# Optimization experiments

Hardware: AMD Instinct MI355X
Metric: run time of the kernel (lower is better)

Reference implementation:

```python
import jax, jax.numpy as jnp
import numpy as np

B, T, C, H = 8, 2048, 1024, 64  # batch, time(block_size), n_embd, head_size


def setup_inputs() -> dict:
    key = jax.random.key(0)
    k1, k2, k3, k4 = jax.random.split(key, 4)
    x = jax.random.normal(k1, (B, T, C), dtype=jnp.float32)
    # nn.Linear(n_embd, head_size, bias=False): y = x @ W.T with W [H, C];
    # store as [C, H] so projection is x @ W.
    Wq = jax.random.normal(k2, (C, H), dtype=jnp.float32) * 0.02
    Wk = jax.random.normal(k3, (C, H), dtype=jnp.float32) * 0.02
    Wv = jax.random.normal(k4, (C, H), dtype=jnp.float32) * 0.02
    return {"x": x, "Wq": Wq, "Wk": Wk, "Wv": Wv}


def reference(x, Wq, Wk, Wv):
    # x: [B, T, C]
    Bb, Tt, Cc = x.shape
    q = x @ Wq  # [B, T, H]
    k = x @ Wk  # [B, T, H]
    v = x @ Wv  # [B, T, H]
    # scores = Q @ K^T / sqrt(channels)  -- note: code scales by n_embd, not head_size
    scale = jnp.asarray(Cc, x.dtype) ** 0.5
    scores = jnp.einsum('bth,bsh->bts', q, k) / scale  # [B, T, T]
    # causal mask (decoder=True): lower-triangular allowed
    causal = jnp.tril(jnp.ones((Tt, Tt), dtype=bool))
    scores = jnp.where(causal, scores, -jnp.inf)
    attn = jax.nn.softmax(scores, axis=-1)  # [B, T, T]
    # dropout p=0.0 -> identity
    res = attn @ v  # [B, T, H]
    return res, attn
```

## Files before the change

### kernel.cpp

```cpp
#include <hip/hip_runtime.h>
#include <hip/hip_bf16.h>


typedef __attribute__((ext_vector_type(8))) short bf16x8;
typedef __attribute__((ext_vector_type(4))) float f32x4;

#define NB 8
#define NT 2048
#define NC 1024
#define NH 64

__device__ __forceinline__ unsigned short f2bf(float f) {
    unsigned int u = __builtin_bit_cast(unsigned int, f);
    u += 0x7fffu + ((u >> 16) & 1u);
    return (unsigned short)(u >> 16);
}

__device__ __forceinline__ bf16x8 cvt8(float4 a, float4 b) {
    union { bf16x8 v; __hip_bfloat162 h[4]; } u;
    u.h[0] = __float22bfloat162_rn(make_float2(a.x, a.y));
    u.h[1] = __float22bfloat162_rn(make_float2(a.z, a.w));
    u.h[2] = __float22bfloat162_rn(make_float2(b.x, b.y));
    u.h[3] = __float22bfloat162_rn(make_float2(b.z, b.w));
    return u.v;
}

__device__ __forceinline__ void async_ld16(const void* g, const void* l) {
    __builtin_amdgcn_global_load_lds(
        (const __attribute__((address_space(1))) unsigned int*)g,
        (__attribute__((address_space(3))) unsigned int*)(unsigned int)(unsigned long long)l,
        16, 0, 0);
}

__global__ __launch_bounds__(256) void wt_kernel(
        const float* __restrict__ Wq,
        const float* __restrict__ Wk,
        const float* __restrict__ Wv,
        unsigned short* __restrict__ Wt) {
    __shared__ float tile[64][65];
    int m  = blockIdx.x >> 4;
    int k0 = (blockIdx.x & 15) * 64;
    const float* W = (m == 0) ? Wq : ((m == 1) ? Wk : Wv);
    int tid = threadIdx.x;
    for (int i = 0; i < 4; ++i) {
        int f = tid + i * 256;
        int r = f >> 4, c4 = (f & 15) * 4;
        float4 v = *(const float4*)&W[(size_t)(k0 + r) * 64 + c4];
        tile[r][c4 + 0] = v.x; tile[r][c4 + 1] = v.y;
        tile[r][c4 + 2] = v.z; tile[r][c4 + 3] = v.w;
    }
    __syncthreads();
    int n  = tid & 63;
    int kq = (tid >> 6) * 16;
    float scale = (m == 0) ? 0.03125f : 1.0f;
    __attribute__((aligned(16))) unsigned short outv[16];
    for (int j = 0; j < 16; ++j)
        outv[j] = f2bf(tile[kq + j][n] * scale);
    unsigned short* dst = &Wt[(size_t)m * (64 * 1024) + (size_t)n * 1024 + k0 + kq];
    *(uint4*)dst       = *(const uint4*)&outv[0];
    *(uint4*)(dst + 8) = *(const uint4*)&outv[8];
}

__global__ __launch_bounds__(256) void qkv_kernel(
        const float* __restrict__ x,
        const unsigned short* __restrict__ Wt,
        unsigned short* __restrict__ qkv,
        unsigned short* __restrict__ v_t) {
    __shared__ float At[32 * 64];
    __shared__ unsigned short Bt[192 * 64];
    char* Ab = (char*)At;
    char* Bb = (char*)Bt;

    int tid  = threadIdx.x;
    int wave = tid >> 6, lane = tid & 63, quad = lane >> 4, l15 = lane & 15;
    int row0 = blockIdx.x * 32;

    f32x4 acc[2][3];
#pragma unroll
    for (int rt = 0; rt < 2; ++rt)
#pragma unroll
        for (int j = 0; j < 3; ++j) acc[rt][j] = (f32x4){0.f, 0.f, 0.f, 0.f};

    for (int kb = 0; kb < 16; ++kb) {
        __syncthreads();
#pragma unroll
        for (int i = 0; i < 2; ++i) {
            int s = i * 256 + tid;
            int m = s >> 4, p = s & 15;
            int j = (p & 8) | ((p & 7) ^ (m & 7));
            async_ld16(x + (size_t)(row0 + m) * NC + kb * 64 + j * 4,
                       Ab + i * 4096 + wave * 1024);
        }
#pragma unroll
        for (int i = 0; i < 6; ++i) {
            int s = i * 256 + tid;
            int n = s >> 3, p = s & 7;
            int j = p ^ (n & 7);
            async_ld16(Wt + (size_t)n * NC + kb * 64 + j * 8,
                       Bb + i * 4096 + wave * 1024);
        }
        __syncthreads();

#pragma unroll
        for (int c = 0; c < 2; ++c) {
            bf16x8 af[2];
#pragma unroll
            for (int rt = 0; rt < 2; ++rt) {
                int m  = rt * 16 + l15;
                int j0 = c * 8 + quad * 2;
                int p0 = (j0 & 8) | ((j0 & 7) ^ (m & 7));
                int p1 = (j0 & 8) | (((j0 + 1) & 7) ^ (m & 7));
                float4 a0 = *(const float4*)(Ab + m * 256 + p0 * 16);
                float4 a1 = *(const float4*)(Ab + m * 256 + p1 * 16);
                af[rt] = cvt8(a0, a1);
            }
#pragma unroll
            for (int jj = 0; jj < 3; ++jj) {
                int n = (wave * 3 + jj) * 16 + l15;
                int p = (c * 4 + quad) ^ (n & 7);
                bf16x8 bf = *(const bf16x8*)(Bb + n * 128 + p * 16);
#pragma unroll
                for (int rt = 0; rt < 2; ++rt)
                    acc[rt][jj] = __builtin_amdgcn_mfma_f32_16x16x32_bf16(
                        af[rt], bf, acc[rt][jj], 0, 0, 0);
            }
        }
    }

    int b = row0 >> 11;
#pragma unroll
    for (int jj = 0; jj < 3; ++jj) {
        int g   = wave * 3 + jj;
        int mat = g >> 2;
        int col = (g & 3) * 16 + l15;
#pragma unroll
        for (int rt = 0; rt < 2; ++rt) {
            int rowb = row0 + rt * 16 + quad * 4;
            if (mat < 2) {
#pragma unroll
                for (int r = 0; r < 4; ++r)
                    qkv[(size_t)mat * (16384 * 64) + (size_t)(rowb + r) * 64 + col] =
                        f2bf(acc[rt][jj][r]);
            } else {
                union { unsigned long long q; unsigned short us[4]; } pk;
#pragma unroll
                for (int r = 0; r < 4; ++r) pk.us[r] = f2bf(acc[rt][jj][r]);
                *(unsigned long long*)&v_t[((size_t)b * 64 + col) * NT + (rowb & 2047)] = pk.q;
            }
        }
    }
}

__global__ __launch_bounds__(256) void lsum_kernel(
        const unsigned short* __restrict__ qg,
        const unsigned short* __restrict__ kg,
        float* __restrict__ l) {
    __shared__ unsigned short kt[64 * 64];
    char* ktb = (char*)kt;
    int tid  = threadIdx.x;
    int wave = tid >> 6, lane = tid & 63, quad = lane >> 4, l15 = lane & 15;
    int it = blockIdx.x >> 2, qq = blockIdx.x & 3;
    int b  = blockIdx.y;
    if (qq > it) return;
    int t0 = it * 64;
    size_t brow = (size_t)b * NT;

    bf16x8 qf[2];
    {
        const unsigned short* qp = qg + (brow + t0 + wave * 16 + l15) * NH + quad * 8;
        qf[0] = *(const bf16x8*)qp;
        qf[1] = *(const bf16x8*)(qp + 32);
    }
    int trow[4];
#pragma unroll
    for (int r = 0; r < 4; ++r) trow[r] = t0 + wave * 16 + quad * 4 + r;

    float rs[4] = {0.f, 0.f, 0.f, 0.f};

    for (int st = qq; st <= it; st += 4) {
        __syncthreads();
#pragma unroll
        for (int i = 0; i < 2; ++i) {
            int s = i * 256 + tid;
            int r = s >> 3, p = s & 7;
            int j = p ^ (r & 7);
            async_ld16(kg + (brow + st * 64 + r) * NH + j * 8,
                       ktb + i * 4096 + wave * 1024);
        }
        __syncthreads();

        f32x4 sacc[4];
#pragma unroll
        for (int nt = 0; nt < 4; ++nt) sacc[nt] = (f32x4){0.f, 0.f, 0.f, 0.f};
#pragma unroll
        for (int c = 0; c < 2; ++c)
#pragma unroll
            for (int nt = 0; nt < 4; ++nt) {
                int n = nt * 16 + l15;
                int p = (c * 4 + quad) ^ (n & 7);
                bf16x8 kf = *(const bf16x8*)(ktb + n * 128 + p * 16);
                sacc[nt] = __builtin_amdgcn_mfma_f32_16x16x32_bf16(qf[c], kf, sacc[nt], 0, 0, 0);
            }
        bool dia = (st == it);
#pragma unroll
        for (int nt = 0; nt < 4; ++nt) {
            int s_g = st * 64 + nt * 16 + l15;
#pragma unroll
            for (int r = 0; r < 4; ++r) {
                float e = __expf(sacc[nt][r]);
                if (dia && s_g > trow[r]) e = 0.f;
                rs[r] += e;
            }
        }
    }
#pragma unroll
    for (int r = 0; r < 4; ++r) {
        float v = rs[r];
        v += __shfl_xor(v, 1, 16);
        v += __shfl_xor(v, 2, 16);
        v += __shfl_xor(v, 4, 16);
        v += __shfl_xor(v, 8, 16);
        if (l15 == 0)
            unsafeAtomicAdd(&l[brow + trow[r]], v);
    }
}

__global__ __launch_bounds__(256) void attn_m_kernel(
        const unsigned short* __restrict__ qg,
        const unsigned short* __restrict__ kg,
        const unsigned short* __restrict__ vtg,
        const float* __restrict__ l,
        float* __restrict__ res,
        float* __restrict__ attn) {
    __shared__ unsigned short kt[64 * 64];
    __shared__ unsigned short vt[64 * 64];
    __shared__ float ptf[4 * 16 * 68];
    char* ktb = (char*)kt;
    char* vtb = (char*)vt;

    int tid  = threadIdx.x;
    int wave = tid >> 6, lane = tid & 63, quad = lane >> 4, l15 = lane & 15;
    int it = blockIdx.x >> 2, qq = blockIdx.x & 3;
    int b  = blockIdx.y;
    if (qq > it) return;
    int t0 = it * 64;
    size_t brow = (size_t)b * NT;

    bf16x8 qf[2];
    {
        const unsigned short* qp = qg + (brow + t0 + wave * 16 + l15) * NH + quad * 8;
        qf[0] = *(const bf16x8*)qp;
        qf[1] = *(const bf16x8*)(qp + 32);
    }
    int trow[4];
    float rinv[4];
#pragma unroll
    for (int r = 0; r < 4; ++r) {
        trow[r] = t0 + wave * 16 + quad * 4 + r;
        rinv[r] = 1.0f / l[brow + trow[r]];
    }

    f32x4 oacc[4];
#pragma unroll
    for (int nt = 0; nt < 4; ++nt) oacc[nt] = (f32x4){0.f, 0.f, 0.f, 0.f};

    for (int st = qq; st <= it; st += 4) {
        __syncthreads();
#pragma unroll
        for (int i = 0; i < 2; ++i) {
            int s = i * 256 + tid;
            int r = s >> 3, p = s & 7;
            int j = p ^ (r & 7);
            async_ld16(kg + (brow + st * 64 + r) * NH + j * 8,
                       ktb + i * 4096 + wave * 1024);
        }
#pragma unroll
        for (int i = 0; i < 2; ++i) {
            int s = i * 256 + tid;
            int r = s >> 3, p = s & 7;
            int j = p ^ (r & 7);
            async_ld16(vtg + ((size_t)b * 64 + r) * NT + st * 64 + j * 8,
                       vtb + i * 4096 + wave * 1024);
        }
        __syncthreads();

        f32x4 sacc[4];
#pragma unroll
        for (int nt = 0; nt < 4; ++nt) sacc[nt] = (f32x4){0.f, 0.f, 0.f, 0.f};
#pragma unroll
        for (int c = 0; c < 2; ++c)
#pragma unroll
            for (int nt = 0; nt < 4; ++nt) {
                int n = nt * 16 + l15;
                int p = (c * 4 + quad) ^ (n & 7);
                bf16x8 kf = *(const bf16x8*)(ktb + n * 128 + p * 16);
                sacc[nt] = __builtin_amdgcn_mfma_f32_16x16x32_bf16(qf[c], kf, sacc[nt], 0, 0, 0);
            }

        bool dia = (st == it);
#pragma unroll
        for (int nt = 0; nt < 4; ++nt) {
            int s_g = st * 64 + nt * 16 + l15;
#pragma unroll
            for (int r = 0; r < 4; ++r) {
                float p = __expf(sacc[nt][r]) * rinv[r];
                if (dia && s_g > trow[r]) p = 0.f;
                ptf[wave * 1088 + (quad * 4 + r) * 68 + nt * 16 + l15] = p;
            }
        }
        asm volatile("s_waitcnt lgkmcnt(0)" ::: "memory");

#pragma unroll
        for (int r = 0; r < 4; ++r) {
            int row = quad * 4 + r;
            float4 pv = *(const float4*)&ptf[wave * 1088 + row * 68 + l15 * 4];
            *(float4*)&attn[(brow + t0 + wave * 16 + row) * NT + st * 64 + l15 * 4] = pv;
        }

#pragma unroll
        for (int c = 0; c < 2; ++c) {
            const float* pp = &ptf[wave * 1088 + l15 * 68 + c * 32 + quad * 8];
            float4 a0 = *(const float4*)pp;
            float4 a1 = *(const float4*)(pp + 4);
            bf16x8 pf = cvt8(a0, a1);
#pragma unroll
            for (int nt = 0; nt < 4; ++nt) {
                int n = nt * 16 + l15;
                int p = (c * 4 + quad) ^ (n & 7);
                bf16x8 vf = *(const bf16x8*)(vtb + n * 128 + p * 16);
                oacc[nt] = __builtin_amdgcn_mfma_f32_16x16x32_bf16(pf, vf, oacc[nt], 0, 0, 0);
            }
        }
    }

#pragma unroll
    for (int nt = 0; nt < 4; ++nt)
#pragma unroll
        for (int r = 0; r < 4; ++r)
            unsafeAtomicAdd(&res[(brow + trow[r]) * NH + nt * 16 + l15], oacc[nt][r]);
}

__global__ __launch_bounds__(256) void zero_kernel(float* __restrict__ attn) {
    int lt = blockIdx.x, b = blockIdx.y;
    float fr = sqrtf(8.f * (float)lt + 1.f);
    int i = (int)((fr + 1.f) * 0.5f);
    while (i * (i - 1) / 2 > lt) --i;
    while ((i + 1) * i / 2 <= lt) ++i;
    int j = lt - i * (i - 1) / 2;
    int it = j, st = i;
    size_t brow = (size_t)b * NT;
    int t0 = it * 64;
    float4 z4 = {0.f, 0.f, 0.f, 0.f};
    int tid = threadIdx.x;
    for (int k = 0; k < 4; ++k) {
        int f = tid + k * 256;
        int r = f >> 4, c4 = (f & 15) * 4;
        *(float4*)&attn[(brow + t0 + r) * NT + st * 64 + c4] = z4;
    }
}

extern "C" void kernel_launch(void* const* d_in, const int* in_sizes, int n_in,
                              void* d_out, int out_size, void* d_ws, size_t ws_size,
                              hipStream_t stream) {
    const float* x  = (const float*)d_in[0];
    const float* Wq = (const float*)d_in[1];
    const float* Wk = (const float*)d_in[2];
    const float* Wv = (const float*)d_in[3];

    unsigned short* ws  = (unsigned short*)d_ws;
    unsigned short* Wt  = ws;
    unsigned short* qkv = ws + 3 * 64 * 1024;
    unsigned short* v_t = qkv + 2 * 16384 * 64;
    float* l = (float*)(v_t + 16384 * 64);

    float* res  = (float*)d_out;
    float* attn = res + (size_t)NB * NT * NH;

    hipMemsetAsync(l, 0, (size_t)NB * NT * sizeof(float), stream);
    hipMemsetAsync(res, 0, (size_t)NB * NT * NH * sizeof(float), stream);

    hipLaunchKernelGGL(wt_kernel, dim3(48), dim3(256), 0, stream, Wq, Wk, Wv, Wt);
    hipLaunchKernelGGL(qkv_kernel, dim3(512), dim3(256), 0, stream, x, Wt, qkv, v_t);

    const unsigned short* qg = qkv;
    const unsigned short* kg = qkv + 16384 * 64;

    hipLaunchKernelGGL(lsum_kernel, dim3(128, 8), dim3(256), 0, stream, qg, kg, l);
    hipLaunchKernelGGL(attn_m_kernel, dim3(128, 8), dim3(256), 0, stream,
                       qg, kg, v_t, l, res, attn);
    hipLaunchKernelGGL(zero_kernel, dim3(496, 8), dim3(256), 0, stream, attn);
}
```

Before: 229.6 us.

## Fuse row-sum and attention passes, normalize attn and output in finalize kernel

Merges the separate row-sum pass and the attention pass into one kernel that writes unnormalized exp scores to attn, accumulates P@V unnormalized, and atomically adds row sums. A new finalize kernel reads the attn lower triangle back, scales it by the inverse row sum, zeros the upper triangle and rescales the output rows. This removes the repeated QK^T and exp work, but adds a full read-modify-write of the lower-triangular attn matrix in global memory. It also relies on no max subtraction, which the previous code already assumed.

```diff
diff --git a/kernel.cpp b/kernel.cpp
--- a/kernel.cpp
+++ b/kernel.cpp
@@ -151,12 +151,19 @@
     }
 }
 
-__global__ __launch_bounds__(256) void lsum_kernel(
+__global__ __launch_bounds__(256) void attn_u_kernel(
         const unsigned short* __restrict__ qg,
         const unsigned short* __restrict__ kg,
-        float* __restrict__ l) {
+        const unsigned short* __restrict__ vtg,
+        float* __restrict__ l,
+        float* __restrict__ res,
+        float* __restrict__ attn) {
     __shared__ unsigned short kt[64 * 64];
+    __shared__ unsigned short vt[64 * 64];
+    __shared__ float ptf[4 * 16 * 68];
     char* ktb = (char*)kt;
+    char* vtb = (char*)vt;
+
     int tid  = threadIdx.x;
     int wave = tid >> 6, lane = tid & 63, quad = lane >> 4, l15 = lane & 15;
     int it = blockIdx.x >> 2, qq = blockIdx.x & 3;
@@ -175,6 +182,9 @@
 #pragma unroll
     for (int r = 0; r < 4; ++r) trow[r] = t0 + wave * 16 + quad * 4 + r;
 
+    f32x4 oacc[4];
+#pragma unroll
+    for (int nt = 0; nt < 4; ++nt) oacc[nt] = (f32x4){0.f, 0.f, 0.f, 0.f};
     float rs[4] = {0.f, 0.f, 0.f, 0.f};
 
     for (int st = qq; st <= it; st += 4) {
@@ -187,6 +197,14 @@
             async_ld16(kg + (brow + st * 64 + r) * NH + j * 8,
                        ktb + i * 4096 + wave * 1024);
         }
+#pragma unroll
+        for (int i = 0; i < 2; ++i) {
+            int s = i * 256 + tid;
+            int r = s >> 3, p = s & 7;
+            int j = p ^ (r & 7);
+            async_ld16(vtg + ((size_t)b * 64 + r) * NT + st * 64 + j * 8,
+                       vtb + i * 4096 + wave * 1024);
+        }
         __syncthreads();
 
         f32x4 sacc[4];
@@ -201,6 +219,7 @@
                 bf16x8 kf = *(const bf16x8*)(ktb + n * 128 + p * 16);
                 sacc[nt] = __builtin_amdgcn_mfma_f32_16x16x32_bf16(qf[c], kf, sacc[nt], 0, 0, 0);
             }
+
         bool dia = (st == it);
 #pragma unroll
         for (int nt = 0; nt < 4; ++nt) {
@@ -210,9 +229,34 @@
                 float e = __expf(sacc[nt][r]);
                 if (dia && s_g > trow[r]) e = 0.f;
                 rs[r] += e;
-            }
-        }
-    }
+                ptf[wave * 1088 + (quad * 4 + r) * 68 + nt * 16 + l15] = e;
+            }
+        }
+        asm volatile("s_waitcnt lgkmcnt(0)" ::: "memory");
+
+#pragma unroll
+        for (int r = 0; r < 4; ++r) {
+            int row = quad * 4 + r;
+            float4 pv = *(const float4*)&ptf[wave * 1088 + row * 68 + l15 * 4];
+            *(float4*)&attn[(brow + t0 + wave * 16 + row) * NT + st * 64 + l15 * 4] = pv;
+        }
+
+#pragma unroll
+        for (int c = 0; c < 2; ++c) {
+            const float* pp = &ptf[wave * 1088 + l15 * 68 + c * 32 + quad * 8];
+            float4 a0 = *(const float4*)pp;
+            float4 a1 = *(const float4*)(pp + 4);
+            bf16x8 pf = cvt8(a0, a1);
+#pragma unroll
+            for (int nt = 0; nt < 4; ++nt) {
+                int n = nt * 16 + l15;
+                int p = (c * 4 + quad) ^ (n & 7);
+                bf16x8 vf = *(const bf16x8*)(vtb + n * 128 + p * 16);
+                oacc[nt] = __builtin_amdgcn_mfma_f32_16x16x32_bf16(pf, vf, oacc[nt], 0, 0, 0);
+            }
+        }
+    }
+
 #pragma unroll
     for (int r = 0; r < 4; ++r) {
         float v = rs[r];
@@ -223,139 +267,62 @@
         if (l15 == 0)
             unsafeAtomicAdd(&l[brow + trow[r]], v);
     }
-}
-
-__global__ __launch_bounds__(256) void attn_m_kernel(
-        const unsigned short* __restrict__ qg,
-        const unsigned short* __restrict__ kg,
-        const unsigned short* __restrict__ vtg,
+
+#pragma unroll
+    for (int nt = 0; nt < 4; ++nt)
+#pragma unroll
+        for (int r = 0; r < 4; ++r)
+            unsafeAtomicAdd(&res[(brow + trow[r]) * NH + nt * 16 + l15], oacc[nt][r]);
+}
+
+__global__ __launch_bounds__(256) void finalize_kernel(
         const float* __restrict__ l,
         float* __restrict__ res,
         float* __restrict__ attn) {
-    __shared__ unsigned short kt[64 * 64];
-    __shared__ unsigned short vt[64 * 64];
-    __shared__ float ptf[4 * 16 * 68];
-    char* ktb = (char*)kt;
-    char* vtb = (char*)vt;
-
-    int tid  = threadIdx.x;
-    int wave = tid >> 6, lane = tid & 63, quad = lane >> 4, l15 = lane & 15;
-    int it = blockIdx.x >> 2, qq = blockIdx.x & 3;
+    __shared__ float rinv[64];
+    int bx = blockIdx.x;
+    int it = bx >> 5, st = bx & 31;
     int b  = blockIdx.y;
-    if (qq > it) return;
-    int t0 = it * 64;
-    size_t brow = (size_t)b * NT;
-
-    bf16x8 qf[2];
-    {
-        const unsigned short* qp = qg + (brow + t0 + wave * 16 + l15) * NH + quad * 8;
-        qf[0] = *(const bf16x8*)qp;
-        qf[1] = *(const bf16x8*)(qp + 32);
-    }
-    int trow[4];
-    float rinv[4];
-#pragma unroll
-    for (int r = 0; r < 4; ++r) {
-        trow[r] = t0 + wave * 16 + quad * 4 + r;
-        rinv[r] = 1.0f / l[brow + trow[r]];
-    }
-
-    f32x4 oacc[4];
-#pragma unroll
-    for (int nt = 0; nt < 4; ++nt) oacc[nt] = (f32x4){0.f, 0.f, 0.f, 0.f};
-
-    for (int st = qq; st <= it; st += 4) {
-        __syncthreads();
-#pragma unroll
-        for (int i = 0; i < 2; ++i) {
-            int s = i * 256 + tid;
-            int r = s >> 3, p = s & 7;
-            int j = p ^ (r & 7);
-            async_ld16(kg + (brow + st * 64 + r) * NH + j * 8,
-                       ktb + i * 4096 + wave * 1024);
-        }
-#pragma unroll
-        for (int i = 0; i < 2; ++i) {
-            int s = i * 256 + tid;
-            int r = s >> 3, p = s & 7;
-            int j = p ^ (r & 7);
-            async_ld16(vtg + ((size_t)b * 64 + r) * NT + st * 64 + j * 8,
-                       vtb + i * 4096 + wave * 1024);
-        }
-        __syncthreads();
-
-        f32x4 sacc[4];
-#pragma unroll
-        for (int nt = 0; nt < 4; ++nt) sacc[nt] = (f32x4){0.f, 0.f, 0.f, 0.f};
-#pragma unroll
-        for (int c = 0; c < 2; ++c)
-#pragma unroll
-            for (int nt = 0; nt < 4; ++nt) {
-                int n = nt * 16 + l15;
-                int p = (c * 4 + quad) ^ (n & 7);
-                bf16x8 kf = *(const bf16x8*)(ktb + n * 128 + p * 16);
-                sacc[nt] = __builtin_amdgcn_mfma_f32_16x16x32_bf16(qf[c], kf, sacc[nt], 0, 0, 0);
-            }
-
-        bool dia = (st == it);
-#pragma unroll
-        for (int nt = 0; nt < 4; ++nt) {
-            int s_g = st * 64 + nt * 16 + l15;
-#pragma unroll
-            for (int r = 0; r < 4; ++r) {
-                float p = __expf(sacc[nt][r]) * rinv[r];
-                if (dia && s_g > trow[r]) p = 0.f;
-                ptf[wave * 1088 + (quad * 4 + r) * 68 + nt * 16 + l15] = p;
-            }
-        }
-        asm volatile("s_waitcnt lgkmcnt(0)" ::: "memory");
-
-#pragma unroll
-        for (int r = 0; r < 4; ++r) {
-            int row = quad * 4 + r;
-            float4 pv = *(const float4*)&ptf[wave * 1088 + row * 68 + l15 * 4];
-            *(float4*)&attn[(brow + t0 + wave * 16 + row) * NT + st * 64 + l15 * 4] = pv;
-        }
-
-#pragma unroll
-        for (int c = 0; c < 2; ++c) {
-            const float* pp = &ptf[wave * 1088 + l15 * 68 + c * 32 + quad * 8];
-            float4 a0 = *(const float4*)pp;
-            float4 a1 = *(const float4*)(pp + 4);
-            bf16x8 pf = cvt8(a0, a1);
-#pragma unroll
-            for (int nt = 0; nt < 4; ++nt) {
-                int n = nt * 16 + l15;
-                int p = (c * 4 + quad) ^ (n & 7);
-                bf16x8 vf = *(const bf16x8*)(vtb + n * 128 + p * 16);
-                oacc[nt] = __builtin_amdgcn_mfma_f32_16x16x32_bf16(pf, vf, oacc[nt], 0, 0, 0);
-            }
-        }
-    }
-
-#pragma unroll
-    for (int nt = 0; nt < 4; ++nt)
-#pragma unroll
-        for (int r = 0; r < 4; ++r)
-            unsafeAtomicAdd(&res[(brow + trow[r]) * NH + nt * 16 + l15], oacc[nt][r]);
-}
-
-__global__ __launch_bounds__(256) void zero_kernel(float* __restrict__ attn) {
-    int lt = blockIdx.x, b = blockIdx.y;
-    float fr = sqrtf(8.f * (float)lt + 1.f);
-    int i = (int)((fr + 1.f) * 0.5f);
-    while (i * (i - 1) / 2 > lt) --i;
-    while ((i + 1) * i / 2 <= lt) ++i;
-    int j = lt - i * (i - 1) / 2;
-    int it = j, st = i;
     size_t brow = (size_t)b * NT;
     int t0 = it * 64;
-    float4 z4 = {0.f, 0.f, 0.f, 0.f};
     int tid = threadIdx.x;
+
+    if (st > it) {
+        float4 z4 = {0.f, 0.f, 0.f, 0.f};
+#pragma unroll
+        for (int k = 0; k < 4; ++k) {
+            int f = tid + k * 256;
+            int r = f >> 4, c4 = (f & 15) * 4;
+            *(float4*)&attn[(brow + t0 + r) * NT + st * 64 + c4] = z4;
+        }
+        return;
+    }
+
+    if (tid < 64) rinv[tid] = 1.0f / l[brow + t0 + tid];
+    __syncthreads();
+
+#pragma unroll
     for (int k = 0; k < 4; ++k) {
         int f = tid + k * 256;
         int r = f >> 4, c4 = (f & 15) * 4;
-        *(float4*)&attn[(brow + t0 + r) * NT + st * 64 + c4] = z4;
+        float* p = &attn[(brow + t0 + r) * NT + st * 64 + c4];
+        float4 v = *(const float4*)p;
+        float s = rinv[r];
+        v.x *= s; v.y *= s; v.z *= s; v.w *= s;
+        *(float4*)p = v;
+    }
+
+    if (st == it) {
+#pragma unroll
+        for (int k = 0; k < 4; ++k) {
+            int f = tid + k * 256;
+            int r = f >> 4, c4 = (f & 15) * 4;
+            float* p = &res[(brow + t0 + r) * NH + c4];
+            float4 v = *(const float4*)p;
+            float s = rinv[r];
+            v.x *= s; v.y *= s; v.z *= s; v.w *= s;
+            *(float4*)p = v;
+        }
     }
 }
 
@@ -385,8 +352,8 @@
     const unsigned short* qg = qkv;
     const unsigned short* kg = qkv + 16384 * 64;
 
-    hipLaunchKernelGGL(lsum_kernel, dim3(128, 8), dim3(256), 0, stream, qg, kg, l);
-    hipLaunchKernelGGL(attn_m_kernel, dim3(128, 8), dim3(256), 0, stream,
+    hipLaunchKernelGGL(attn_u_kernel, dim3(128, 8), dim3(256), 0, stream,
                        qg, kg, v_t, l, res, attn);
-    hipLaunchKernelGGL(zero_kernel, dim3(496, 8), dim3(256), 0, stream, attn);
-}
+    hipLaunchKernelGGL(finalize_kernel, dim3(1024, 8), dim3(256), 0, stream,
+                       l, res, attn);
+}
```

Result: slower. 236.3 us (+2.9%).

## Double-buffer LDS tiles in QKV, row-sum and attention kernels

Applied to the files above, without the earlier changes.

Adds two-stage LDS ping-pong buffering to the QKV projection, the softmax row-sum and the attention output kernels. The next K/V (or x/W) tile is prefetched with async global-to-LDS loads while the current tile feeds the MFMAs, and the second barrier per iteration is dropped. The aim is to hide global load latency behind matrix math. In exchange, LDS use doubles (64 KB per block in the QKV kernel), which can lower occupancy. The full vmcnt(0) drain also waits on outstanding attn stores.

```diff
diff --git a/kernel.cpp b/kernel.cpp
--- a/kernel.cpp
+++ b/kernel.cpp
@@ -9,6 +9,8 @@
 #define NT 2048
 #define NC 1024
 #define NH 64
+
+#define VM_DRAIN() asm volatile("s_waitcnt vmcnt(0)" ::: "memory")
 
 __device__ __forceinline__ unsigned short f2bf(float f) {
     unsigned int u = __builtin_bit_cast(unsigned int, f);
@@ -66,10 +68,7 @@
         const unsigned short* __restrict__ Wt,
         unsigned short* __restrict__ qkv,
         unsigned short* __restrict__ v_t) {
-    __shared__ float At[32 * 64];
-    __shared__ unsigned short Bt[192 * 64];
-    char* Ab = (char*)At;
-    char* Bb = (char*)Bt;
+    __shared__ char smem[65536];
 
     int tid  = threadIdx.x;
     int wave = tid >> 6, lane = tid & 63, quad = lane >> 4, l15 = lane & 15;
@@ -81,26 +80,48 @@
 #pragma unroll
         for (int j = 0; j < 3; ++j) acc[rt][j] = (f32x4){0.f, 0.f, 0.f, 0.f};
 
+#pragma unroll
+    for (int i = 0; i < 2; ++i) {
+        int s = i * 256 + tid;
+        int m = s >> 4, p = s & 15;
+        int j = (p & 8) | ((p & 7) ^ (m & 7));
+        async_ld16(x + (size_t)(row0 + m) * NC + j * 4,
+                   smem + i * 4096 + wave * 1024);
+    }
+#pragma unroll
+    for (int i = 0; i < 6; ++i) {
+        int s = i * 256 + tid;
+        int n = s >> 3, p = s & 7;
+        int j = p ^ (n & 7);
+        async_ld16(Wt + (size_t)n * NC + j * 8,
+                   smem + 8192 + i * 4096 + wave * 1024);
+    }
+
+    int cur = 0;
     for (int kb = 0; kb < 16; ++kb) {
+        VM_DRAIN();
         __syncthreads();
-#pragma unroll
-        for (int i = 0; i < 2; ++i) {
-            int s = i * 256 + tid;
-            int m = s >> 4, p = s & 15;
-            int j = (p & 8) | ((p & 7) ^ (m & 7));
-            async_ld16(x + (size_t)(row0 + m) * NC + kb * 64 + j * 4,
-                       Ab + i * 4096 + wave * 1024);
-        }
-#pragma unroll
-        for (int i = 0; i < 6; ++i) {
-            int s = i * 256 + tid;
-            int n = s >> 3, p = s & 7;
-            int j = p ^ (n & 7);
-            async_ld16(Wt + (size_t)n * NC + kb * 64 + j * 8,
-                       Bb + i * 4096 + wave * 1024);
-        }
-        __syncthreads();
-
+        if (kb < 15) {
+            char* nb = smem + (cur ^ 1) * 32768;
+#pragma unroll
+            for (int i = 0; i < 2; ++i) {
+                int s = i * 256 + tid;
+                int m = s >> 4, p = s & 15;
+                int j = (p & 8) | ((p & 7) ^ (m & 7));
+                async_ld16(x + (size_t)(row0 + m) * NC + (kb + 1) * 64 + j * 4,
+                           nb + i * 4096 + wave * 1024);
+            }
+#pragma unroll
+            for (int i = 0; i < 6; ++i) {
+                int s = i * 256 + tid;
+                int n = s >> 3, p = s & 7;
+                int j = p ^ (n & 7);
+                async_ld16(Wt + (size_t)n * NC + (kb + 1) * 64 + j * 8,
+                           nb + 8192 + i * 4096 + wave * 1024);
+            }
+        }
+        char* Ab = smem + cur * 32768;
+        char* Bb = Ab + 8192;
 #pragma unroll
         for (int c = 0; c < 2; ++c) {
             bf16x8 af[2];
@@ -125,6 +146,7 @@
                         af[rt], bf, acc[rt][jj], 0, 0, 0);
             }
         }
+        cur ^= 1;
     }
 
     int b = row0 >> 11;
@@ -155,7 +177,7 @@
         const unsigned short* __restrict__ qg,
         const unsigned short* __restrict__ kg,
         float* __restrict__ l) {
-    __shared__ unsigned short kt[64 * 64];
+    __shared__ unsigned short kt[2 * 64 * 64];
     char* ktb = (char*)kt;
     int tid  = threadIdx.x;
     int wave = tid >> 6, lane = tid & 63, quad = lane >> 4, l15 = lane & 15;
@@ -175,19 +197,32 @@
 #pragma unroll
     for (int r = 0; r < 4; ++r) trow[r] = t0 + wave * 16 + quad * 4 + r;
 
+#pragma unroll
+    for (int i = 0; i < 2; ++i) {
+        int s = i * 256 + tid;
+        int r = s >> 3, p = s & 7;
+        int j = p ^ (r & 7);
+        async_ld16(kg + (brow + qq * 64 + r) * NH + j * 8,
+                   ktb + i * 4096 + wave * 1024);
+    }
+
     float rs[4] = {0.f, 0.f, 0.f, 0.f};
+    int cur = 0;
 
     for (int st = qq; st <= it; st += 4) {
+        VM_DRAIN();
         __syncthreads();
-#pragma unroll
-        for (int i = 0; i < 2; ++i) {
-            int s = i * 256 + tid;
-            int r = s >> 3, p = s & 7;
-            int j = p ^ (r & 7);
-            async_ld16(kg + (brow + st * 64 + r) * NH + j * 8,
-                       ktb + i * 4096 + wave * 1024);
-        }
-        __syncthreads();
+        if (st + 4 <= it) {
+#pragma unroll
+            for (int i = 0; i < 2; ++i) {
+                int s = i * 256 + tid;
+                int r = s >> 3, p = s & 7;
+                int j = p ^ (r & 7);
+                async_ld16(kg + (brow + (st + 4) * 64 + r) * NH + j * 8,
+                           ktb + (cur ^ 1) * 8192 + i * 4096 + wave * 1024);
+            }
+        }
+        char* kb = ktb + cur * 8192;
 
         f32x4 sacc[4];
 #pragma unroll
@@ -198,7 +233,7 @@
             for (int nt = 0; nt < 4; ++nt) {
                 int n = nt * 16 + l15;
                 int p = (c * 4 + quad) ^ (n & 7);
-                bf16x8 kf = *(const bf16x8*)(ktb + n * 128 + p * 16);
+                bf16x8 kf = *(const bf16x8*)(kb + n * 128 + p * 16);
                 sacc[nt] = __builtin_amdgcn_mfma_f32_16x16x32_bf16(qf[c], kf, sacc[nt], 0, 0, 0);
             }
         bool dia = (st == it);
@@ -212,6 +247,7 @@
                 rs[r] += e;
             }
         }
+        cur ^= 1;
     }
 #pragma unroll
     for (int r = 0; r < 4; ++r) {
@@ -232,8 +268,8 @@
         const float* __restrict__ l,
         float* __restrict__ res,
         float* __restrict__ attn) {
-    __shared__ unsigned short kt[64 * 64];
-    __shared__ unsigned short vt[64 * 64];
+    __shared__ unsigned short kt[2 * 64 * 64];
+    __shared__ unsigned short vt[2 * 64 * 64];
     __shared__ float ptf[4 * 16 * 68];
     char* ktb = (char*)kt;
     char* vtb = (char*)vt;
@@ -264,25 +300,35 @@
 #pragma unroll
     for (int nt = 0; nt < 4; ++nt) oacc[nt] = (f32x4){0.f, 0.f, 0.f, 0.f};
 
+#pragma unroll
+    for (int i = 0; i < 2; ++i) {
+        int s = i * 256 + tid;
+        int r = s >> 3, p = s & 7;
+        int j = p ^ (r & 7);
+        async_ld16(kg + (brow + qq * 64 + r) * NH + j * 8,
+                   ktb + i * 4096 + wave * 1024);
+        async_ld16(vtg + ((size_t)b * 64 + r) * NT + qq * 64 + j * 8,
+                   vtb + i * 4096 + wave * 1024);
+    }
+
+    int cur = 0;
     for (int st = qq; st <= it; st += 4) {
+        VM_DRAIN();
         __syncthreads();
-#pragma unroll
-        for (int i = 0; i < 2; ++i) {
-            int s = i * 256 + tid;
-            int r = s >> 3, p = s & 7;
-            int j = p ^ (r & 7);
-            async_ld16(kg + (brow + st * 64 + r) * NH + j * 8,
-                       ktb + i * 4096 + wave * 1024);
-        }
-#pragma unroll
-        for (int i = 0; i < 2; ++i) {
-            int s = i * 256 + tid;
-            int r = s >> 3, p = s & 7;
-            int j = p ^ (r & 7);
-            async_ld16(vtg + ((size_t)b * 64 + r) * NT + st * 64 + j * 8,
-                       vtb + i * 4096 + wave * 1024);
-        }
-        __syncthreads();
+        if (st + 4 <= it) {
+#pragma unroll
+            for (int i = 0; i < 2; ++i) {
+                int s = i * 256 + tid;
+                int r = s >> 3, p = s & 7;
+                int j = p ^ (r & 7);
+                async_ld16(kg + (brow + (st + 4) * 64 + r) * NH + j * 8,
+                           ktb + (cur ^ 1) * 8192 + i * 4096 + wave * 1024);
+                async_ld16(vtg + ((size_t)b * 64 + r) * NT + (st + 4) * 64 + j * 8,
+                           vtb + (cur ^ 1) * 8192 + i * 4096 + wave * 1024);
+            }
+        }
+        char* kb = ktb + cur * 8192;
+        char* vb = vtb + cur * 8192;
 
         f32x4 sacc[4];
 #pragma unroll
@@ -293,7 +339,7 @@
             for (int nt = 0; nt < 4; ++nt) {
                 int n = nt * 16 + l15;
                 int p = (c * 4 + quad) ^ (n & 7);
-                bf16x8 kf = *(const bf16x8*)(ktb + n * 128 + p * 16);
+                bf16x8 kf = *(const bf16x8*)(kb + n * 128 + p * 16);
                 sacc[nt] = __builtin_amdgcn_mfma_f32_16x16x32_bf16(qf[c], kf, sacc[nt], 0, 0, 0);
             }
 
@@ -327,10 +373,11 @@
             for (int nt = 0; nt < 4; ++nt) {
                 int n = nt * 16 + l15;
                 int p = (c * 4 + quad) ^ (n & 7);
-                bf16x8 vf = *(const bf16x8*)(vtb + n * 128 + p * 16);
+                bf16x8 vf = *(const bf16x8*)(vb + n * 128 + p * 16);
                 oacc[nt] = __builtin_amdgcn_mfma_f32_16x16x32_bf16(pf, vf, oacc[nt], 0, 0, 0);
             }
         }
+        cur ^= 1;
     }
 
 #pragma unroll
```

After: 230.1 us. Within noise of the previous version (+0.3%).
